# Optimization experiments

Measured on AMD Instinct MI355X. Metric: run time of the kernel, lower is better.

## Reference

```python
import jax, jax.numpy as jnp
import numpy as np

N_NODES = 50000
N_EDGES = 200000
D = 128
LN_EPS = 1e-5


def _layer_norm(x, g, b):
    mu = jnp.mean(x, axis=-1, keepdims=True)
    var = jnp.mean(jnp.square(x - mu), axis=-1, keepdims=True)
    return (x - mu) * jax.lax.rsqrt(var + LN_EPS) * g + b


def _mlp(x, W1, b1, W2, b2, W3, b3, g, beta):
    # 2 hidden ReLU layers + linear output + LayerNorm (MeshGraphNets style)
    h = jax.nn.relu(x @ W1 + b1)
    h = jax.nn.relu(h @ W2 + b2)
    h = h @ W3 + b3
    return _layer_norm(h, g, beta)


def setup_inputs() -> dict:
    key = jax.random.key(0)
    ks = jax.random.split(key, 12)
    d = {}
    d["node_features"] = jax.random.normal(ks[0], (N_NODES, D), dtype=jnp.float32)
    d["edge_features"] = jax.random.normal(ks[1], (N_EDGES, D), dtype=jnp.float32)
    d["senders"] = jax.random.randint(ks[2], (N_EDGES,), 0, N_NODES, dtype=jnp.int32)
    d["receivers"] = jax.random.randint(ks[3], (N_EDGES,), 0, N_NODES, dtype=jnp.int32)
    def lin(k, fan_in, fan_out):
        return jax.random.normal(k, (fan_in, fan_out), dtype=jnp.float32) / np.sqrt(fan_in)
    # edge MLP: [3D] -> D -> D -> D
    d["We1"] = lin(ks[4], 3 * D, D); d["be1"] = jnp.zeros((D,), jnp.float32)
    d["We2"] = lin(ks[5], D, D);     d["be2"] = jnp.zeros((D,), jnp.float32)
    d["We3"] = lin(ks[6], D, D);     d["be3"] = jnp.zeros((D,), jnp.float32)
    d["ge"] = jnp.ones((D,), jnp.float32); d["bege"] = jnp.zeros((D,), jnp.float32)
    # node MLP: [2D] -> D -> D -> D
    d["Wn1"] = lin(ks[7], 2 * D, D); d["bn1"] = jnp.zeros((D,), jnp.float32)
    d["Wn2"] = lin(ks[8], D, D);     d["bn2"] = jnp.zeros((D,), jnp.float32)
    d["Wn3"] = lin(ks[9], D, D);     d["bn3"] = jnp.zeros((D,), jnp.float32)
    d["gn"] = jnp.ones((D,), jnp.float32); d["begn"] = jnp.zeros((D,), jnp.float32)
    return d


def reference(node_features, edge_features, senders, receivers,
              We1, be1, We2, be2, We3, be3, ge, bege,
              Wn1, bn1, Wn2, bn2, Wn3, bn3, gn, begn):
    num_nodes = node_features.shape[0]
    # --- edge update: gather sender/receiver feats, concat, edge MLP ---
    edge_in = jnp.concatenate(
        [node_features[senders], node_features[receivers], edge_features], axis=-1)  # [E, 3D]
    new_edge = _mlp(edge_in, We1, be1, We2, be2, We3, be3, ge, bege)  # [E, D]
    # --- node update: scatter-sum aggregate, concat, node MLP ---
    agg = jax.ops.segment_sum(new_edge, receivers, num_segments=num_nodes)  # [N, D]
    node_in = jnp.concatenate([node_features, agg], axis=-1)  # [N, 2D]
    new_node = _mlp(node_in, Wn1, bn1, Wn2, bn2, Wn3, bn3, gn, begn)
    # --- residuals ---
    new_node = new_node + node_features
    new_edge = new_edge + edge_features
    return new_node, new_edge
```

## Files before the change

kernel.cpp:

```cpp
#include <hip/hip_runtime.h>

#define NNODES 50000
#define NEDGES 200000
#define DD 128
#define LN_EPS 1e-5f
#define NTH 256

typedef __attribute__((ext_vector_type(8))) short bf16x8;
typedef __attribute__((ext_vector_type(4))) float f32x4;
typedef __attribute__((ext_vector_type(16))) float f32x16;

template<int N> struct ic { static constexpr int value = N; };

__device__ __forceinline__ unsigned short bfr(float f) {
    union { float f; unsigned u; } v; v.f = f;
    return (unsigned short)((v.u + 0x7fffu + ((v.u >> 16) & 1u)) >> 16);
}
__device__ __forceinline__ unsigned pk2(float a, float b) {
    return (unsigned)bfr(a) | ((unsigned)bfr(b) << 16);
}
__device__ __forceinline__ void gload_lds16(const void* g, void* l) {
    __builtin_amdgcn_global_load_lds(
        (const __attribute__((address_space(1))) void*)g,
        (__attribute__((address_space(3))) void*)l, 16, 0, 0);
}

__global__ void build_wimg(const float* __restrict__ We1, const float* __restrict__ We2,
                           const float* __restrict__ We3, const float* __restrict__ Wn1,
                           const float* __restrict__ Wn2, const float* __restrict__ Wn3,
                           char* __restrict__ img_e, char* __restrict__ img_n) {
    int tid = blockIdx.x * NTH + threadIdx.x;
    const float* W; char* dst; int q;
    if      (tid <  6144) { W = We1; dst = img_e;             q = tid;         }
    else if (tid <  8192) { W = We2; dst = img_e + 12 * 8192; q = tid - 6144;  }
    else if (tid < 10240) { W = We3; dst = img_e + 16 * 8192; q = tid - 8192;  }
    else if (tid < 14336) { W = Wn1; dst = img_n;             q = tid - 10240; }
    else if (tid < 16384) { W = Wn2; dst = img_n + 8 * 8192;  q = tid - 14336; }
    else if (tid < 18432) { W = Wn3; dst = img_n + 12 * 8192; q = tid - 16384; }
    else return;
    int c = q >> 9, rem = q & 511;
    int nt = rem >> 7, r2 = rem & 127, n32 = r2 >> 2, ks = r2 & 3;
    int n = nt * 32 + n32;
    int sx = (n32 + (n32 >> 2)) & 3;
    int k0 = c * 32 + ks * 8;
    unsigned short o[8];
    #pragma unroll
    for (int e = 0; e < 8; ++e)
        o[e] = bfr(W[(size_t)(k0 + e) * DD + n]);
    uint4 val;
    val.x = (unsigned)o[0] | ((unsigned)o[1] << 16);
    val.y = (unsigned)o[2] | ((unsigned)o[3] << 16);
    val.z = (unsigned)o[4] | ((unsigned)o[5] << 16);
    val.w = (unsigned)o[6] | ((unsigned)o[7] << 16);
    *(uint4*)(dst + (size_t)c * 8192 + nt * 2048 + n32 * 64 + ((ks ^ sx) << 4)) = val;
}

__global__ __launch_bounds__(NTH)
void cvt_histo(const float* __restrict__ nodef, const int* __restrict__ recv,
               uint4* __restrict__ nodb, int* __restrict__ cnt) {
    const int tid0 = blockIdx.x * NTH + threadIdx.x;
    if (tid0 < NEDGES) atomicAdd(&cnt[recv[tid0]], 1);
    const int NG = NNODES * 16;
    for (int g = tid0; g < NG; g += gridDim.x * NTH) {
        f32x4 a = ((const f32x4*)nodef)[g * 2];
        f32x4 b = ((const f32x4*)nodef)[g * 2 + 1];
        uint4 o;
        o.x = pk2(a[0], a[1]); o.y = pk2(a[2], a[3]);
        o.z = pk2(b[0], b[1]); o.w = pk2(b[2], b[3]);
        nodb[g] = o;
    }
}

__global__ __launch_bounds__(NTH)
void csr_scan1(const int* __restrict__ cnt, int* __restrict__ part) {
    __shared__ int red[NTH];
    const int b = blockIdx.x, t = threadIdx.x;
    const int base = b * 196;
    int s = 0;
    for (int i = t; i < 196; i += NTH) {
        int idx = base + i;
        if (idx < NNODES) s += cnt[idx];
    }
    red[t] = s;
    __syncthreads();
    for (int d = NTH / 2; d > 0; d >>= 1) {
        if (t < d) red[t] += red[t + d];
        __syncthreads();
    }
    if (t == 0) part[b] = red[0];
}

__global__ __launch_bounds__(NTH)
void csr_scan2(const int* __restrict__ cnt, const int* __restrict__ part,
               int* __restrict__ off, int* __restrict__ cursor) {
    __shared__ int sp[NTH];
    const int t = threadIdx.x;
    sp[t] = part[t];
    __syncthreads();
    for (int d = 1; d < NTH; d <<= 1) {
        int v = (t >= d) ? sp[t - d] : 0;
        __syncthreads();
        sp[t] += v;
        __syncthreads();
    }
    int run = (t == 0) ? 0 : sp[t - 1];
    const int base = t * 196;
    for (int i = 0; i < 196; ++i) {
        int idx = base + i;
        if (idx < NNODES) { off[idx] = run; cursor[idx] = run; run += cnt[idx]; }
    }
    if (t == NTH - 1) off[NNODES] = NEDGES;
}

__global__ void csr_fill(const int* __restrict__ recv, int* __restrict__ cursor,
                         int* __restrict__ perm) {
    int e = blockIdx.x * NTH + threadIdx.x;
    if (e < NEDGES) {
        int p = atomicAdd(&cursor[recv[e]], 1);
        perm[e] = p;
    }
}

__global__ __launch_bounds__(NTH)
void aggregate(const unsigned* __restrict__ ybuf,
               const int* __restrict__ off,
               unsigned* __restrict__ aggb) {
    const int n = blockIdx.x * 4 + (threadIdx.x >> 6);
    const int l = threadIdx.x & 63;
    if (n >= NNODES) return;
    const int j0 = off[n], j1 = off[n + 1];
    float sx = 0.f, sy = 0.f;
    int j = j0;
    for (; j + 4 <= j1; j += 4) {
        unsigned v0 = ybuf[(size_t)j * 64 + l];
        unsigned v1 = ybuf[(size_t)(j + 1) * 64 + l];
        unsigned v2 = ybuf[(size_t)(j + 2) * 64 + l];
        unsigned v3 = ybuf[(size_t)(j + 3) * 64 + l];
        sx += __uint_as_float(v0 << 16) + __uint_as_float(v1 << 16)
            + __uint_as_float(v2 << 16) + __uint_as_float(v3 << 16);
        sy += __uint_as_float(v0 & 0xffff0000u) + __uint_as_float(v1 & 0xffff0000u)
            + __uint_as_float(v2 & 0xffff0000u) + __uint_as_float(v3 & 0xffff0000u);
    }
    for (; j < j1; ++j) {
        unsigned v = ybuf[(size_t)j * 64 + l];
        sx += __uint_as_float(v << 16);
        sy += __uint_as_float(v & 0xffff0000u);
    }
    aggb[(size_t)n * 64 + l] = pk2(sx, sy);
}

template<int MODE>
__global__ __launch_bounds__(NTH, 2)
void mgn_mfma(const float* __restrict__ nodef, const float* __restrict__ edgef,
              const unsigned short* __restrict__ nodb,
              const int* __restrict__ senders, const int* __restrict__ receivers,
              const int* __restrict__ perm,
              const char* __restrict__ img,
              const float* __restrict__ b1, const float* __restrict__ b2,
              const float* __restrict__ b3,
              const float* __restrict__ gamma, const float* __restrict__ beta,
              const unsigned short* __restrict__ aggb, unsigned* __restrict__ ybuf,
              float* __restrict__ outp)
{
    __shared__ char Wbuf[5 * 8192];
    __shared__ char Hb[4 * 8192];

    const int t  = threadIdx.x;
    const int w  = t >> 6;
    const int l  = t & 63;
    const int ln = l & 31;
    const int hi = l >> 5;
    const int row0 = blockIdx.x * 128;
    const int gm = row0 + w * 32 + ln;
    constexpr int NROWS = (MODE == 0) ? NEDGES : NNODES;
    constexpr int NK1   = (MODE == 0) ? 12 : 8;
    constexpr int NCH   = NK1 + 8;
    const int gmc = gm < NROWS ? gm : NROWS - 1;
    const int sxA = (ln + (ln >> 2)) & 3;
    const int sxH = ln & 15;

    int srow = 0, rrow = 0, prow = 0;
    if (MODE == 0) { srow = senders[gmc]; rrow = receivers[gmc]; prow = perm[gmc]; }

    const f32x16 fz = {0.f,0.f,0.f,0.f,0.f,0.f,0.f,0.f,
                       0.f,0.f,0.f,0.f,0.f,0.f,0.f,0.f};
    f32x16 acc[4];
    #pragma unroll
    for (int nt = 0; nt < 4; ++nt) acc[nt] = fz;

    bf16x8 bS[3][2];
    f32x4  fS[3][4];

    auto stageW = [&](int c) {
        const char* src = img + (size_t)c * 8192 + t * 16;
        char* dstl = Wbuf + (c % 5) * 8192 + t * 16;
        gload_lds16(src, dstl);
        gload_lds16(src + 4096, dstl + 4096);
    };

    auto loadBB = [&](auto CC, bf16x8* dst) {
        constexpr int c = decltype(CC)::value;
        const unsigned short* base;
        if constexpr (MODE == 0) {
            base = (c < 4) ? nodb + (size_t)srow * DD : nodb + (size_t)rrow * DD;
        } else {
            base = (c < 4) ? nodb + (size_t)gmc * DD : aggb + (size_t)gmc * DD;
        }
        const char* p = (const char*)base + (c & 3) * 64 + hi * 16;
        dst[0] = *(const bf16x8*)p;
        dst[1] = *(const bf16x8*)(p + 32);
    };

    auto loadBF = [&](auto CC, f32x4* dst) {
        constexpr int c = decltype(CC)::value;
        const float* p = edgef + (size_t)gmc * DD + (c & 3) * 32 + hi * 8;
        dst[0] = *(const f32x4*)p;
        dst[1] = *(const f32x4*)(p + 4);
        dst[2] = *(const f32x4*)(p + 16);
        dst[3] = *(const f32x4*)(p + 20);
    };

    auto cvtB = [&](const f32x4* br) {
        union { unsigned u[4]; bf16x8 v; } r;
        r.u[0] = pk2(br[0][0], br[0][1]);
        r.u[1] = pk2(br[0][2], br[0][3]);
        r.u[2] = pk2(br[1][0], br[1][1]);
        r.u[3] = pk2(br[1][2], br[1][3]);
        return r.v;
    };

    auto loadBH = [&](int ks, int kh) {
        const char* p = Hb + w * 8192 + ln * 256
                      + (((ks * 4 + kh * 2 + hi) ^ sxH) << 4);
        return *(const bf16x8*)p;
    };

    auto getB = [&](auto CC, int kh) -> bf16x8 {
        constexpr int c = decltype(CC)::value;
        if constexpr (c >= NK1) {
            return loadBH((c - NK1) & 3, kh);
        } else if constexpr (MODE == 0 && c >= 8) {
            return cvtB(&fS[c % 3][kh * 2]);
        } else {
            return bS[c % 3][kh];
        }
    };

    auto compute = [&](auto CC) {
        constexpr int c = decltype(CC)::value;
        const char* bp = Wbuf + (c % 5) * 8192 + ln * 64;
        #pragma unroll
        for (int kh = 0; kh < 2; ++kh) {
            bf16x8 b = getB(CC, kh);
            #pragma unroll
            for (int nt = 0; nt < 4; ++nt) {
                bf16x8 a = *(const bf16x8*)(bp + nt * 2048
                            + (((kh * 2 + hi) ^ sxA) << 4));
                acc[nt] = __builtin_amdgcn_mfma_f32_32x32x16_bf16(a, b, acc[nt], 0, 0, 0);
            }
        }
    };

    auto epiH = [&](const float* bias) {
        #pragma unroll
        for (int nt = 0; nt < 4; ++nt) {
            #pragma unroll
            for (int rq = 0; rq < 4; ++rq) {
                f32x4 bv = *(const f32x4*)(bias + nt * 32 + rq * 8 + hi * 4);
                unsigned short h[4];
                #pragma unroll
                for (int j = 0; j < 4; ++j)
                    h[j] = bfr(fmaxf(acc[nt][rq * 4 + j] + bv[j], 0.f));
                char* p = Hb + w * 8192 + ln * 256
                        + (((nt * 4 + rq) ^ sxH) << 4) + hi * 8;
                unsigned lo = (unsigned)h[0] | ((unsigned)h[1] << 16);
                unsigned hx = (unsigned)h[2] | ((unsigned)h[3] << 16);
                *(unsigned long long*)p =
                    (unsigned long long)lo | ((unsigned long long)hx << 32);
            }
            acc[nt] = fz;
        }
    };

#define PITER(C, VM)                                                          \
    {                                                                         \
        if constexpr ((C) + 3 < NCH) stageW((C) + 3);                         \
        __builtin_amdgcn_sched_barrier(0);                                    \
        if constexpr ((C) + 2 < NK1) {                                        \
            if constexpr (MODE == 0 && (C) + 2 >= 8)                          \
                loadBF(ic<(C) + 2>{}, fS[((C) + 2) % 3]);                     \
            else                                                              \
                loadBB(ic<(C) + 2>{}, bS[((C) + 2) % 3]);                     \
        }                                                                     \
        __builtin_amdgcn_sched_barrier(0);                                    \
        asm volatile("s_waitcnt vmcnt(" #VM ")" ::: "memory");                \
        __builtin_amdgcn_sched_barrier(0);                                    \
        __builtin_amdgcn_s_barrier();                                         \
        __builtin_amdgcn_sched_barrier(0);                                    \
        compute(ic<(C)>{});                                                   \
    }

    stageW(0);
    __builtin_amdgcn_sched_barrier(0);
    loadBB(ic<0>{}, bS[0]);
    __builtin_amdgcn_sched_barrier(0);
    stageW(1);
    __builtin_amdgcn_sched_barrier(0);
    loadBB(ic<1>{}, bS[1]);
    __builtin_amdgcn_sched_barrier(0);
    stageW(2);
    __builtin_amdgcn_sched_barrier(0);

    if constexpr (MODE == 0) {
        PITER(0, 12)  PITER(1, 12)  PITER(2, 12)  PITER(3, 14)
        PITER(4, 14)  PITER(5, 14)  PITER(6, 14)  PITER(7, 14)
        PITER(8, 14)  PITER(9, 14)  PITER(10, 12) PITER(11, 10)
        epiH(b1);
        PITER(12, 8)  PITER(13, 6)  PITER(14, 6)  PITER(15, 6)
        epiH(b2);
        PITER(16, 6)  PITER(17, 4)  PITER(18, 2)  PITER(19, 0)
    } else {
        PITER(0, 12)  PITER(1, 12)  PITER(2, 12)  PITER(3, 14)
        PITER(4, 14)  PITER(5, 14)  PITER(6, 12)  PITER(7, 10)
        epiH(b1);
        PITER(8, 8)   PITER(9, 6)   PITER(10, 6)  PITER(11, 6)
        epiH(b2);
        PITER(12, 6)  PITER(13, 4)  PITER(14, 2)  PITER(15, 0)
    }
#undef PITER

    float vsum = 0.f, vsq = 0.f;
    #pragma unroll
    for (int nt = 0; nt < 4; ++nt) {
        #pragma unroll
        for (int rq = 0; rq < 4; ++rq) {
            f32x4 bv = *(const f32x4*)(b3 + nt * 32 + rq * 8 + hi * 4);
            #pragma unroll
            for (int j = 0; j < 4; ++j) {
                float v = acc[nt][rq * 4 + j] + bv[j];
                acc[nt][rq * 4 + j] = v;
                vsum += v; vsq += v * v;
            }
        }
    }
    vsum += __shfl_xor(vsum, 32);
    vsq  += __shfl_xor(vsq, 32);
    const float mu = vsum * (1.f / DD);
    const float rs = rsqrtf(vsq * (1.f / DD) - mu * mu + LN_EPS);

    if (gm < NROWS) {
        const float* resid = ((MODE == 0) ? edgef : nodef) + (size_t)gm * DD;
        #pragma unroll
        for (int nt = 0; nt < 4; ++nt) {
            #pragma unroll
            for (int rq = 0; rq < 4; ++rq) {
                const int n0 = nt * 32 + rq * 8 + hi * 4;
                f32x4 gv = *(const f32x4*)(gamma + n0);
                f32x4 bv = *(const f32x4*)(beta + n0);
                f32x4 rv = *(const f32x4*)(resid + n0);
                float y[4];
                f32x4 o;
                #pragma unroll
                for (int j = 0; j < 4; ++j) {
                    y[j] = (acc[nt][rq * 4 + j] - mu) * rs * gv[j] + bv[j];
                    o[j] = y[j] + rv[j];
                }
                *(f32x4*)(outp + (size_t)gm * DD + n0) = o;
                if (MODE == 0) {
                    unsigned long long pkd =
                        (unsigned long long)pk2(y[0], y[1])
                      | ((unsigned long long)pk2(y[2], y[3]) << 32);
                    *(unsigned long long*)((char*)ybuf + (size_t)prow * 256 + n0 * 2) = pkd;
                }
            }
        }
    }
}

extern "C" void kernel_launch(void* const* d_in, const int* in_sizes, int n_in,
                              void* d_out, int out_size, void* d_ws, size_t ws_size,
                              hipStream_t stream) {
    const float* nodef = (const float*)d_in[0];
    const float* edgef = (const float*)d_in[1];
    const int* senders   = (const int*)d_in[2];
    const int* receivers = (const int*)d_in[3];
    const float* We1 = (const float*)d_in[4],  *be1 = (const float*)d_in[5];
    const float* We2 = (const float*)d_in[6],  *be2 = (const float*)d_in[7];
    const float* We3 = (const float*)d_in[8],  *be3 = (const float*)d_in[9];
    const float* ge  = (const float*)d_in[10], *bege = (const float*)d_in[11];
    const float* Wn1 = (const float*)d_in[12], *bn1 = (const float*)d_in[13];
    const float* Wn2 = (const float*)d_in[14], *bn2 = (const float*)d_in[15];
    const float* Wn3 = (const float*)d_in[16], *bn3 = (const float*)d_in[17];
    const float* gn  = (const float*)d_in[18], *begn = (const float*)d_in[19];

    float* out_node = (float*)d_out;
    float* out_edge = (float*)d_out + (size_t)NNODES * DD;

    char* ws = (char*)d_ws;
    size_t o = 0;
    unsigned short* aggb = (unsigned short*)(ws + o); o += (size_t)NNODES * 256;
    unsigned* ybuf = (unsigned*)(ws + o);             o += (size_t)NEDGES * 256;
    unsigned short* nodb = (unsigned short*)(ws + o); o += (size_t)NNODES * 256;
    char* img_e = ws + o;           o += 20 * 8192;
    char* img_n = ws + o;           o += 16 * 8192;
    int* cnt    = (int*)(ws + o);   o += NNODES * 4;
    int* cursor = (int*)(ws + o);   o += NNODES * 4;
    int* off    = (int*)(ws + o);   o += (NNODES + 4) * 4;
    int* part   = (int*)(ws + o);   o += NTH * 4;
    int* perm   = (int*)(ws + o);   o += NEDGES * 4;

    hipMemsetAsync(cnt, 0, NNODES * 4, stream);
    cvt_histo<<<1024, NTH, 0, stream>>>(nodef, receivers, (uint4*)nodb, cnt);
    build_wimg<<<72, NTH, 0, stream>>>(We1, We2, We3, Wn1, Wn2, Wn3, img_e, img_n);
    csr_scan1<<<NTH, NTH, 0, stream>>>(cnt, part);
    csr_scan2<<<1, NTH, 0, stream>>>(cnt, part, off, cursor);
    csr_fill<<<(NEDGES + NTH - 1) / NTH, NTH, 0, stream>>>(receivers, cursor, perm);

    mgn_mfma<0><<<dim3((NEDGES + 127) / 128), dim3(NTH), 0, stream>>>(
        nodef, edgef, nodb, senders, receivers, perm, img_e,
        be1, be2, be3, ge, bege, aggb, ybuf, out_edge);

    aggregate<<<(NNODES + 3) / 4, NTH, 0, stream>>>(ybuf, off, (unsigned*)aggb);

    mgn_mfma<1><<<dim3((NNODES + 127) / 128), dim3(NTH), 0, stream>>>(
        nodef, edgef, nodb, senders, receivers, perm, img_n,
        bn1, bn2, bn3, gn, begn, aggb, ybuf, out_node);
}
```

Before: 316.3 us.

## Process two K-chunks per barrier with deeper weight staging and merge prepass kernels

Restructures the MFMA main loop so each pipeline step stages two weight chunks, loads two activation chunks and computes two chunks per workgroup barrier. The LDS weight ring grows from 5 to 6 slots and the register operand buffers from 3 to 4, halving the number of barriers and increasing prefetch distance. It also merges the weight-image build and node conversion/histogram kernels into one launch to save a kernel launch. The cost is more LDS and register pressure at 2 waves per SIMD, which may hurt occupancy or cause spills.

```diff
diff --git a/kernel.cpp b/kernel.cpp
--- a/kernel.cpp
+++ b/kernel.cpp
@@ -25,49 +25,51 @@
         (__attribute__((address_space(3))) void*)l, 16, 0, 0);
 }
 
-__global__ void build_wimg(const float* __restrict__ We1, const float* __restrict__ We2,
-                           const float* __restrict__ We3, const float* __restrict__ Wn1,
-                           const float* __restrict__ Wn2, const float* __restrict__ Wn3,
-                           char* __restrict__ img_e, char* __restrict__ img_n) {
-    int tid = blockIdx.x * NTH + threadIdx.x;
-    const float* W; char* dst; int q;
-    if      (tid <  6144) { W = We1; dst = img_e;             q = tid;         }
-    else if (tid <  8192) { W = We2; dst = img_e + 12 * 8192; q = tid - 6144;  }
-    else if (tid < 10240) { W = We3; dst = img_e + 16 * 8192; q = tid - 8192;  }
-    else if (tid < 14336) { W = Wn1; dst = img_n;             q = tid - 10240; }
-    else if (tid < 16384) { W = Wn2; dst = img_n + 8 * 8192;  q = tid - 14336; }
-    else if (tid < 18432) { W = Wn3; dst = img_n + 12 * 8192; q = tid - 16384; }
-    else return;
-    int c = q >> 9, rem = q & 511;
-    int nt = rem >> 7, r2 = rem & 127, n32 = r2 >> 2, ks = r2 & 3;
-    int n = nt * 32 + n32;
-    int sx = (n32 + (n32 >> 2)) & 3;
-    int k0 = c * 32 + ks * 8;
-    unsigned short o[8];
-    #pragma unroll
-    for (int e = 0; e < 8; ++e)
-        o[e] = bfr(W[(size_t)(k0 + e) * DD + n]);
-    uint4 val;
-    val.x = (unsigned)o[0] | ((unsigned)o[1] << 16);
-    val.y = (unsigned)o[2] | ((unsigned)o[3] << 16);
-    val.z = (unsigned)o[4] | ((unsigned)o[5] << 16);
-    val.w = (unsigned)o[6] | ((unsigned)o[7] << 16);
-    *(uint4*)(dst + (size_t)c * 8192 + nt * 2048 + n32 * 64 + ((ks ^ sx) << 4)) = val;
-}
-
 __global__ __launch_bounds__(NTH)
-void cvt_histo(const float* __restrict__ nodef, const int* __restrict__ recv,
-               uint4* __restrict__ nodb, int* __restrict__ cnt) {
-    const int tid0 = blockIdx.x * NTH + threadIdx.x;
-    if (tid0 < NEDGES) atomicAdd(&cnt[recv[tid0]], 1);
-    const int NG = NNODES * 16;
-    for (int g = tid0; g < NG; g += gridDim.x * NTH) {
-        f32x4 a = ((const f32x4*)nodef)[g * 2];
-        f32x4 b = ((const f32x4*)nodef)[g * 2 + 1];
-        uint4 o;
-        o.x = pk2(a[0], a[1]); o.y = pk2(a[2], a[3]);
-        o.z = pk2(b[0], b[1]); o.w = pk2(b[2], b[3]);
-        nodb[g] = o;
+void prepass(const float* __restrict__ We1, const float* __restrict__ We2,
+             const float* __restrict__ We3, const float* __restrict__ Wn1,
+             const float* __restrict__ Wn2, const float* __restrict__ Wn3,
+             char* __restrict__ img_e, char* __restrict__ img_n,
+             const float* __restrict__ nodef, const int* __restrict__ recv,
+             uint4* __restrict__ nodb, int* __restrict__ cnt) {
+    if (blockIdx.x < 72) {
+        int tid = blockIdx.x * NTH + threadIdx.x;
+        const float* W; char* dst; int q;
+        if      (tid <  6144) { W = We1; dst = img_e;             q = tid;         }
+        else if (tid <  8192) { W = We2; dst = img_e + 12 * 8192; q = tid - 6144;  }
+        else if (tid < 10240) { W = We3; dst = img_e + 16 * 8192; q = tid - 8192;  }
+        else if (tid < 14336) { W = Wn1; dst = img_n;             q = tid - 10240; }
+        else if (tid < 16384) { W = Wn2; dst = img_n + 8 * 8192;  q = tid - 14336; }
+        else if (tid < 18432) { W = Wn3; dst = img_n + 12 * 8192; q = tid - 16384; }
+        else return;
+        int c = q >> 9, rem = q & 511;
+        int nt = rem >> 7, r2 = rem & 127, n32 = r2 >> 2, ks = r2 & 3;
+        int n = nt * 32 + n32;
+        int sx = (n32 + (n32 >> 2)) & 3;
+        int k0 = c * 32 + ks * 8;
+        unsigned short o[8];
+        #pragma unroll
+        for (int e = 0; e < 8; ++e)
+            o[e] = bfr(W[(size_t)(k0 + e) * DD + n]);
+        uint4 val;
+        val.x = (unsigned)o[0] | ((unsigned)o[1] << 16);
+        val.y = (unsigned)o[2] | ((unsigned)o[3] << 16);
+        val.z = (unsigned)o[4] | ((unsigned)o[5] << 16);
+        val.w = (unsigned)o[6] | ((unsigned)o[7] << 16);
+        *(uint4*)(dst + (size_t)c * 8192 + nt * 2048 + n32 * 64 + ((ks ^ sx) << 4)) = val;
+    } else {
+        const int b = blockIdx.x - 72;
+        const int tid0 = b * NTH + threadIdx.x;
+        if (tid0 < NEDGES) atomicAdd(&cnt[recv[tid0]], 1);
+        const int NG = NNODES * 16;
+        for (int g = tid0; g < NG; g += 1024 * NTH) {
+            f32x4 a = ((const f32x4*)nodef)[g * 2];
+            f32x4 bb = ((const f32x4*)nodef)[g * 2 + 1];
+            uint4 o;
+            o.x = pk2(a[0], a[1]); o.y = pk2(a[2], a[3]);
+            o.z = pk2(bb[0], bb[1]); o.w = pk2(bb[2], bb[3]);
+            nodb[g] = o;
+        }
     }
 }
 
@@ -162,7 +164,7 @@
               const unsigned short* __restrict__ aggb, unsigned* __restrict__ ybuf,
               float* __restrict__ outp)
 {
-    __shared__ char Wbuf[5 * 8192];
+    __shared__ char Wbuf[6 * 8192];
     __shared__ char Hb[4 * 8192];
 
     const int t  = threadIdx.x;
@@ -188,12 +190,12 @@
     #pragma unroll
     for (int nt = 0; nt < 4; ++nt) acc[nt] = fz;
 
-    bf16x8 bS[3][2];
-    f32x4  fS[3][4];
+    bf16x8 bS[4][2];
+    f32x4  fS[4][4];
 
     auto stageW = [&](int c) {
         const char* src = img + (size_t)c * 8192 + t * 16;
-        char* dstl = Wbuf + (c % 5) * 8192 + t * 16;
+        char* dstl = Wbuf + (c % 6) * 8192 + t * 16;
         gload_lds16(src, dstl);
         gload_lds16(src + 4096, dstl + 4096);
     };
@@ -240,15 +242,15 @@
         if constexpr (c >= NK1) {
             return loadBH((c - NK1) & 3, kh);
         } else if constexpr (MODE == 0 && c >= 8) {
-            return cvtB(&fS[c % 3][kh * 2]);
+            return cvtB(&fS[c & 3][kh * 2]);
         } else {
-            return bS[c % 3][kh];
+            return bS[c & 3][kh];
         }
     };
 
     auto compute = [&](auto CC) {
         constexpr int c = decltype(CC)::value;
-        const char* bp = Wbuf + (c % 5) * 8192 + ln * 64;
+        const char* bp = Wbuf + (c % 6) * 8192 + ln * 64;
         #pragma unroll
         for (int kh = 0; kh < 2; ++kh) {
             bf16x8 b = getB(CC, kh);
@@ -282,52 +284,57 @@
         }
     };
 
-#define PITER(C, VM)                                                          \
+    auto loadB = [&](auto CC) {
+        constexpr int c = decltype(CC)::value;
+        if constexpr (c < NK1) {
+            if constexpr (MODE == 0 && c >= 8) loadBF(CC, fS[c & 3]);
+            else                               loadBB(CC, bS[c & 3]);
+        }
+    };
+
+#define PITER2(M, VM)                                                         \
     {                                                                         \
-        if constexpr ((C) + 3 < NCH) stageW((C) + 3);                         \
+        __builtin_amdgcn_s_barrier();                                         \
         __builtin_amdgcn_sched_barrier(0);                                    \
-        if constexpr ((C) + 2 < NK1) {                                        \
-            if constexpr (MODE == 0 && (C) + 2 >= 8)                          \
-                loadBF(ic<(C) + 2>{}, fS[((C) + 2) % 3]);                     \
-            else                                                              \
-                loadBB(ic<(C) + 2>{}, bS[((C) + 2) % 3]);                     \
-        }                                                                     \
+        if constexpr (2*(M) + 4 < NCH) stageW(2*(M) + 4);                     \
+        if constexpr (2*(M) + 5 < NCH) stageW(2*(M) + 5);                     \
+        __builtin_amdgcn_sched_barrier(0);                                    \
+        loadB(ic<2*(M) + 2>{});                                               \
+        loadB(ic<2*(M) + 3>{});                                               \
         __builtin_amdgcn_sched_barrier(0);                                    \
         asm volatile("s_waitcnt vmcnt(" #VM ")" ::: "memory");                \
         __builtin_amdgcn_sched_barrier(0);                                    \
-        __builtin_amdgcn_s_barrier();                                         \
-        __builtin_amdgcn_sched_barrier(0);                                    \
-        compute(ic<(C)>{});                                                   \
+        compute(ic<2*(M)>{});                                                 \
+        compute(ic<2*(M) + 1>{});                                             \
     }
 
     stageW(0);
-    __builtin_amdgcn_sched_barrier(0);
-    loadBB(ic<0>{}, bS[0]);
     __builtin_amdgcn_sched_barrier(0);
     stageW(1);
     __builtin_amdgcn_sched_barrier(0);
-    loadBB(ic<1>{}, bS[1]);
-    __builtin_amdgcn_sched_barrier(0);
     stageW(2);
     __builtin_amdgcn_sched_barrier(0);
+    stageW(3);
+    __builtin_amdgcn_sched_barrier(0);
+    loadB(ic<0>{});
+    loadB(ic<1>{});
+    __builtin_amdgcn_sched_barrier(0);
 
     if constexpr (MODE == 0) {
-        PITER(0, 12)  PITER(1, 12)  PITER(2, 12)  PITER(3, 14)
-        PITER(4, 14)  PITER(5, 14)  PITER(6, 14)  PITER(7, 14)
-        PITER(8, 14)  PITER(9, 14)  PITER(10, 12) PITER(11, 10)
+        PITER2(0, 16)  PITER2(1, 20)  PITER2(2, 20)  PITER2(3, 24)
+        PITER2(4, 28)  PITER2(5, 24)
         epiH(b1);
-        PITER(12, 8)  PITER(13, 6)  PITER(14, 6)  PITER(15, 6)
+        PITER2(6, 16)  PITER2(7, 8)
         epiH(b2);
-        PITER(16, 6)  PITER(17, 4)  PITER(18, 2)  PITER(19, 0)
+        PITER2(8, 4)   PITER2(9, 0)
     } else {
-        PITER(0, 12)  PITER(1, 12)  PITER(2, 12)  PITER(3, 14)
-        PITER(4, 14)  PITER(5, 14)  PITER(6, 12)  PITER(7, 10)
+        PITER2(0, 16)  PITER2(1, 20)  PITER2(2, 20)  PITER2(3, 16)
         epiH(b1);
-        PITER(8, 8)   PITER(9, 6)   PITER(10, 6)  PITER(11, 6)
+        PITER2(4, 12)  PITER2(5, 8)
         epiH(b2);
-        PITER(12, 6)  PITER(13, 4)  PITER(14, 2)  PITER(15, 0)
-    }
-#undef PITER
+        PITER2(6, 4)   PITER2(7, 0)
+    }
+#undef PITER2
 
     float vsum = 0.f, vsq = 0.f;
     #pragma unroll
@@ -410,8 +417,9 @@
     int* perm   = (int*)(ws + o);   o += NEDGES * 4;
 
     hipMemsetAsync(cnt, 0, NNODES * 4, stream);
-    cvt_histo<<<1024, NTH, 0, stream>>>(nodef, receivers, (uint4*)nodb, cnt);
-    build_wimg<<<72, NTH, 0, stream>>>(We1, We2, We3, Wn1, Wn2, Wn3, img_e, img_n);
+    prepass<<<72 + 1024, NTH, 0, stream>>>(We1, We2, We3, Wn1, Wn2, Wn3,
+                                           img_e, img_n,
+                                           nodef, receivers, (uint4*)nodb, cnt);
     csr_scan1<<<NTH, NTH, 0, stream>>>(cnt, part);
     csr_scan2<<<1, NTH, 0, stream>>>(cnt, part, off, cursor);
     csr_fill<<<(NEDGES + NTH - 1) / NTH, NTH, 0, stream>>>(receivers, cursor, perm);
```

Result: no change. 311.9 us (-1.4%).

## Keep hidden activations in registers via lane shuffles, drop LDS buffer, merge prepass kernels

Applied to the files above, without the earlier changes.

Hidden-layer activations no longer round-trip through a 32 KB shared-memory buffer. They are packed to bf16 in registers and rearranged into MFMA B-operand fragments with cross-half-wave shuffles. With less LDS per block, the launch bound goes from 2 to 4 blocks per CU to raise occupancy, which risks register spills because the hfr fragments add pressure. The weight-image build and the node-conversion/histogram kernels are also fused into one launch to save a kernel launch.

```diff
diff --git a/kernel.cpp b/kernel.cpp
--- a/kernel.cpp
+++ b/kernel.cpp
@@ -25,49 +25,51 @@
         (__attribute__((address_space(3))) void*)l, 16, 0, 0);
 }
 
-__global__ void build_wimg(const float* __restrict__ We1, const float* __restrict__ We2,
-                           const float* __restrict__ We3, const float* __restrict__ Wn1,
-                           const float* __restrict__ Wn2, const float* __restrict__ Wn3,
-                           char* __restrict__ img_e, char* __restrict__ img_n) {
-    int tid = blockIdx.x * NTH + threadIdx.x;
-    const float* W; char* dst; int q;
-    if      (tid <  6144) { W = We1; dst = img_e;             q = tid;         }
-    else if (tid <  8192) { W = We2; dst = img_e + 12 * 8192; q = tid - 6144;  }
-    else if (tid < 10240) { W = We3; dst = img_e + 16 * 8192; q = tid - 8192;  }
-    else if (tid < 14336) { W = Wn1; dst = img_n;             q = tid - 10240; }
-    else if (tid < 16384) { W = Wn2; dst = img_n + 8 * 8192;  q = tid - 14336; }
-    else if (tid < 18432) { W = Wn3; dst = img_n + 12 * 8192; q = tid - 16384; }
-    else return;
-    int c = q >> 9, rem = q & 511;
-    int nt = rem >> 7, r2 = rem & 127, n32 = r2 >> 2, ks = r2 & 3;
-    int n = nt * 32 + n32;
-    int sx = (n32 + (n32 >> 2)) & 3;
-    int k0 = c * 32 + ks * 8;
-    unsigned short o[8];
-    #pragma unroll
-    for (int e = 0; e < 8; ++e)
-        o[e] = bfr(W[(size_t)(k0 + e) * DD + n]);
-    uint4 val;
-    val.x = (unsigned)o[0] | ((unsigned)o[1] << 16);
-    val.y = (unsigned)o[2] | ((unsigned)o[3] << 16);
-    val.z = (unsigned)o[4] | ((unsigned)o[5] << 16);
-    val.w = (unsigned)o[6] | ((unsigned)o[7] << 16);
-    *(uint4*)(dst + (size_t)c * 8192 + nt * 2048 + n32 * 64 + ((ks ^ sx) << 4)) = val;
-}
-
 __global__ __launch_bounds__(NTH)
-void cvt_histo(const float* __restrict__ nodef, const int* __restrict__ recv,
-               uint4* __restrict__ nodb, int* __restrict__ cnt) {
-    const int tid0 = blockIdx.x * NTH + threadIdx.x;
-    if (tid0 < NEDGES) atomicAdd(&cnt[recv[tid0]], 1);
-    const int NG = NNODES * 16;
-    for (int g = tid0; g < NG; g += gridDim.x * NTH) {
-        f32x4 a = ((const f32x4*)nodef)[g * 2];
-        f32x4 b = ((const f32x4*)nodef)[g * 2 + 1];
-        uint4 o;
-        o.x = pk2(a[0], a[1]); o.y = pk2(a[2], a[3]);
-        o.z = pk2(b[0], b[1]); o.w = pk2(b[2], b[3]);
-        nodb[g] = o;
+void prepass(const float* __restrict__ We1, const float* __restrict__ We2,
+             const float* __restrict__ We3, const float* __restrict__ Wn1,
+             const float* __restrict__ Wn2, const float* __restrict__ Wn3,
+             char* __restrict__ img_e, char* __restrict__ img_n,
+             const float* __restrict__ nodef, const int* __restrict__ recv,
+             uint4* __restrict__ nodb, int* __restrict__ cnt) {
+    if (blockIdx.x < 72) {
+        int tid = blockIdx.x * NTH + threadIdx.x;
+        const float* W; char* dst; int q;
+        if      (tid <  6144) { W = We1; dst = img_e;             q = tid;         }
+        else if (tid <  8192) { W = We2; dst = img_e + 12 * 8192; q = tid - 6144;  }
+        else if (tid < 10240) { W = We3; dst = img_e + 16 * 8192; q = tid - 8192;  }
+        else if (tid < 14336) { W = Wn1; dst = img_n;             q = tid - 10240; }
+        else if (tid < 16384) { W = Wn2; dst = img_n + 8 * 8192;  q = tid - 14336; }
+        else if (tid < 18432) { W = Wn3; dst = img_n + 12 * 8192; q = tid - 16384; }
+        else return;
+        int c = q >> 9, rem = q & 511;
+        int nt = rem >> 7, r2 = rem & 127, n32 = r2 >> 2, ks = r2 & 3;
+        int n = nt * 32 + n32;
+        int sx = (n32 + (n32 >> 2)) & 3;
+        int k0 = c * 32 + ks * 8;
+        unsigned short o[8];
+        #pragma unroll
+        for (int e = 0; e < 8; ++e)
+            o[e] = bfr(W[(size_t)(k0 + e) * DD + n]);
+        uint4 val;
+        val.x = (unsigned)o[0] | ((unsigned)o[1] << 16);
+        val.y = (unsigned)o[2] | ((unsigned)o[3] << 16);
+        val.z = (unsigned)o[4] | ((unsigned)o[5] << 16);
+        val.w = (unsigned)o[6] | ((unsigned)o[7] << 16);
+        *(uint4*)(dst + (size_t)c * 8192 + nt * 2048 + n32 * 64 + ((ks ^ sx) << 4)) = val;
+    } else {
+        const int b = blockIdx.x - 72;
+        const int tid0 = b * NTH + threadIdx.x;
+        if (tid0 < NEDGES) atomicAdd(&cnt[recv[tid0]], 1);
+        const int NG = NNODES * 16;
+        for (int g = tid0; g < NG; g += 1024 * NTH) {
+            f32x4 a = ((const f32x4*)nodef)[g * 2];
+            f32x4 bb = ((const f32x4*)nodef)[g * 2 + 1];
+            uint4 o;
+            o.x = pk2(a[0], a[1]); o.y = pk2(a[2], a[3]);
+            o.z = pk2(bb[0], bb[1]); o.w = pk2(bb[2], bb[3]);
+            nodb[g] = o;
+        }
     }
 }
 
@@ -150,7 +152,7 @@
 }
 
 template<int MODE>
-__global__ __launch_bounds__(NTH, 2)
+__global__ __launch_bounds__(NTH, 4)
 void mgn_mfma(const float* __restrict__ nodef, const float* __restrict__ edgef,
               const unsigned short* __restrict__ nodb,
               const int* __restrict__ senders, const int* __restrict__ receivers,
@@ -163,7 +165,6 @@
               float* __restrict__ outp)
 {
     __shared__ char Wbuf[5 * 8192];
-    __shared__ char Hb[4 * 8192];
 
     const int t  = threadIdx.x;
     const int w  = t >> 6;
@@ -177,7 +178,6 @@
     constexpr int NCH   = NK1 + 8;
     const int gmc = gm < NROWS ? gm : NROWS - 1;
     const int sxA = (ln + (ln >> 2)) & 3;
-    const int sxH = ln & 15;
 
     int srow = 0, rrow = 0, prow = 0;
     if (MODE == 0) { srow = senders[gmc]; rrow = receivers[gmc]; prow = perm[gmc]; }
@@ -190,6 +190,7 @@
 
     bf16x8 bS[3][2];
     f32x4  fS[3][4];
+    bf16x8 hfr[8];
 
     auto stageW = [&](int c) {
         const char* src = img + (size_t)c * 8192 + t * 16;
@@ -229,16 +230,10 @@
         return r.v;
     };
 
-    auto loadBH = [&](int ks, int kh) {
-        const char* p = Hb + w * 8192 + ln * 256
-                      + (((ks * 4 + kh * 2 + hi) ^ sxH) << 4);
-        return *(const bf16x8*)p;
-    };
-
     auto getB = [&](auto CC, int kh) -> bf16x8 {
         constexpr int c = decltype(CC)::value;
         if constexpr (c >= NK1) {
-            return loadBH((c - NK1) & 3, kh);
+            return hfr[((c - NK1) & 3) * 2 + kh];
         } else if constexpr (MODE == 0 && c >= 8) {
             return cvtB(&fS[c % 3][kh * 2]);
         } else {
@@ -261,24 +256,35 @@
         }
     };
 
-    auto epiH = [&](const float* bias) {
+    auto epiR = [&](const float* bias) {
         #pragma unroll
         for (int nt = 0; nt < 4; ++nt) {
+            float rf[16];
             #pragma unroll
             for (int rq = 0; rq < 4; ++rq) {
                 f32x4 bv = *(const f32x4*)(bias + nt * 32 + rq * 8 + hi * 4);
-                unsigned short h[4];
                 #pragma unroll
                 for (int j = 0; j < 4; ++j)
-                    h[j] = bfr(fmaxf(acc[nt][rq * 4 + j] + bv[j], 0.f));
-                char* p = Hb + w * 8192 + ln * 256
-                        + (((nt * 4 + rq) ^ sxH) << 4) + hi * 8;
-                unsigned lo = (unsigned)h[0] | ((unsigned)h[1] << 16);
-                unsigned hx = (unsigned)h[2] | ((unsigned)h[3] << 16);
-                *(unsigned long long*)p =
-                    (unsigned long long)lo | ((unsigned long long)hx << 32);
+                    rf[rq * 4 + j] = fmaxf(acc[nt][rq * 4 + j] + bv[j], 0.f);
             }
             acc[nt] = fz;
+            #pragma unroll
+            for (int kh = 0; kh < 2; ++kh) {
+                const int qo = (2 * kh + hi) * 4;
+                const int qs = (2 * kh + (1 - hi)) * 4;
+                unsigned own0 = pk2(rf[qo],     rf[qo + 1]);
+                unsigned own1 = pk2(rf[qo + 2], rf[qo + 3]);
+                unsigned snd0 = pk2(rf[qs],     rf[qs + 1]);
+                unsigned snd1 = pk2(rf[qs + 2], rf[qs + 3]);
+                unsigned rcv0 = (unsigned)__shfl_xor((int)snd0, 32);
+                unsigned rcv1 = (unsigned)__shfl_xor((int)snd1, 32);
+                union { unsigned u[4]; bf16x8 v; } r;
+                r.u[0] = hi ? rcv0 : own0;
+                r.u[1] = hi ? rcv1 : own1;
+                r.u[2] = hi ? own0 : rcv0;
+                r.u[3] = hi ? own1 : rcv1;
+                hfr[nt * 2 + kh] = r.v;
+            }
         }
     };
 
@@ -315,16 +321,16 @@
         PITER(0, 12)  PITER(1, 12)  PITER(2, 12)  PITER(3, 14)
         PITER(4, 14)  PITER(5, 14)  PITER(6, 14)  PITER(7, 14)
         PITER(8, 14)  PITER(9, 14)  PITER(10, 12) PITER(11, 10)
-        epiH(b1);
+        epiR(b1);
         PITER(12, 8)  PITER(13, 6)  PITER(14, 6)  PITER(15, 6)
-        epiH(b2);
+        epiR(b2);
         PITER(16, 6)  PITER(17, 4)  PITER(18, 2)  PITER(19, 0)
     } else {
         PITER(0, 12)  PITER(1, 12)  PITER(2, 12)  PITER(3, 14)
         PITER(4, 14)  PITER(5, 14)  PITER(6, 12)  PITER(7, 10)
-        epiH(b1);
+        epiR(b1);
         PITER(8, 8)   PITER(9, 6)   PITER(10, 6)  PITER(11, 6)
-        epiH(b2);
+        epiR(b2);
         PITER(12, 6)  PITER(13, 4)  PITER(14, 2)  PITER(15, 0)
     }
 #undef PITER
@@ -410,8 +416,9 @@
     int* perm   = (int*)(ws + o);   o += NEDGES * 4;
 
     hipMemsetAsync(cnt, 0, NNODES * 4, stream);
-    cvt_histo<<<1024, NTH, 0, stream>>>(nodef, receivers, (uint4*)nodb, cnt);
-    build_wimg<<<72, NTH, 0, stream>>>(We1, We2, We3, Wn1, Wn2, Wn3, img_e, img_n);
+    prepass<<<72 + 1024, NTH, 0, stream>>>(We1, We2, We3, Wn1, Wn2, Wn3,
+                                           img_e, img_n,
+                                           nodef, receivers, (uint4*)nodb, cnt);
     csr_scan1<<<NTH, NTH, 0, stream>>>(cnt, part);
     csr_scan2<<<1, NTH, 0, stream>>>(cnt, part, off, cursor);
     csr_fill<<<(NEDGES + NTH - 1) / NTH, NTH, 0, stream>>>(receivers, cursor, perm);
```

Result: slower. 395.3 us (+25.0%).
